# Kernel optimization log

Measured on AMD Instinct MI355X. Metric: run time of the kernel, lower is better.

Reference implementation:

```python
import jax, jax.numpy as jnp
import numpy as np

L, B, H = 1024, 64, 128


def _gru_cell(x, h, wih, whh, bih, bhh):
    # torch.nn.GRUCell math: gates ordered (r, z, n)
    gi = x @ wih.T + bih  # [B, 3H]
    gh = h @ whh.T + bhh  # [B, 3H]
    ir, iz, inn = jnp.split(gi, 3, axis=1)
    hr, hz, hn = jnp.split(gh, 3, axis=1)
    r = jax.nn.sigmoid(ir + hr)
    z = jax.nn.sigmoid(iz + hz)
    n = jnp.tanh(inn + r * hn)
    return (1.0 - z) * n + z * h


def setup_inputs() -> dict:
    key = jax.random.key(0)
    ks = jax.random.split(key, 20)
    s = 0.05  # keep tanh/sigmoid unsaturated
    f32 = jnp.float32
    return {
        "passEnc": jax.random.normal(ks[0], (L, B, 2 * H), f32),
        "Wp_w": jax.random.normal(ks[1], (H, 2 * H), f32) * s,
        "Wp_b": jax.random.normal(ks[2], (H,), f32) * s,
        "Wph_w": jax.random.normal(ks[3], (H, 2 * H), f32) * s,
        "Wph_b": jax.random.normal(ks[4], (H,), f32) * s,
        "Wg_w": jax.random.normal(ks[5], (4 * H, 4 * H), f32) * s,
        "Wg_b": jax.random.normal(ks[6], (4 * H,), f32) * s,
        "Vt": jax.random.normal(ks[7], (B, H, 1), f32),
        "wih_f": jax.random.normal(ks[8], (3 * H, 4 * H), f32) * s,
        "whh_f": jax.random.normal(ks[9], (3 * H, H), f32) * s,
        "bih_f": jax.random.normal(ks[10], (3 * H,), f32) * s,
        "bhh_f": jax.random.normal(ks[11], (3 * H,), f32) * s,
        "wih_r": jax.random.normal(ks[12], (3 * H, 4 * H), f32) * s,
        "whh_r": jax.random.normal(ks[13], (3 * H, H), f32) * s,
        "bih_r": jax.random.normal(ks[14], (3 * H,), f32) * s,
        "bhh_r": jax.random.normal(ks[15], (3 * H,), f32) * s,
        "h0_fwd": jax.random.normal(ks[16], (B, H), f32),
        "h0_rev": jax.random.normal(ks[17], (B, H), f32),
    }


def reference(passEnc, Wp_w, Wp_b, Wph_w, Wph_b, Wg_w, Wg_b, Vt,
              wih_f, whh_f, bih_f, bhh_f, wih_r, whh_r, bih_r, bhh_r,
              h0_fwd, h0_rev):
    v = Vt[:, :, 0]                       # [B, H]
    WPf = passEnc @ Wp_w.T + Wp_b        # loop-invariant WP_sub_v(passEnc), [L, B, H]
    pe_rev = jnp.flip(passEnc, axis=0)
    WPr = jnp.flip(WPf, axis=0)          # linear commutes with flip

    def attend(x_t, WP, pe):
        # x_t: [B, 2H]; WP: [L, B, H]; pe: [L, B, 2H]
        temp = jnp.tanh(WP + x_t @ Wph_w.T + Wph_b)      # [L, B, H]
        scores = jnp.einsum('lbh,bh->bl', temp, v)       # per-batch Vt
        a = jax.nn.softmax(scores, axis=1)               # over L
        c = jnp.einsum('bl,lbd->bd', a, pe)              # [B, 2H]
        cc = jnp.concatenate([x_t, c], axis=1)           # [B, 4H]
        g = jax.nn.sigmoid(cc @ Wg_w.T + Wg_b)
        return g * cc

    def step(carry, xs):
        hf, hr = carry
        xf, xr = xs
        cf = attend(xf, WPf, passEnc)
        cr = attend(xr, WPr, pe_rev)
        hf = _gru_cell(cf, hf, wih_f, whh_f, bih_f, bhh_f)
        hr = _gru_cell(cr, hr, wih_r, whh_r, bih_r, bhh_r)
        return (hf, hr), jnp.concatenate([hf, hr], axis=1)

    _, out = jax.lax.scan(step, (h0_fwd, h0_rev), (passEnc, pe_rev))
    # original applies Dropout(p=0.2); identity in eval mode
    return out  # [L, B, 2H]
```

## Files before the change

kernel.cpp:

```cpp
#include <hip/hip_runtime.h>
#include <hip/hip_bf16.h>

#define DEV __device__ __forceinline__
typedef unsigned short u16;
typedef short bf16x8 __attribute__((ext_vector_type(8)));
typedef float f32x4  __attribute__((ext_vector_type(4)));

static constexpr float LOG2E = 1.44269504088896340736f;
static constexpr float C2E   = 2.88539008177792681472f;

DEV float rcpf_(float x){ return __builtin_amdgcn_rcpf(x); }
DEV float exp2f_(float x){ return __builtin_amdgcn_exp2f(x); }
DEV float sigmoidf_(float x){ return rcpf_(1.f + exp2f_(-LOG2E*x)); }
DEV float tanhf_fast(float x){ return 1.f - 2.f*rcpf_(exp2f_(C2E*x) + 1.f); }
DEV u16 bfu(float f){
  __hip_bfloat16 h = __float2bfloat16(f);
  union { __hip_bfloat16 h; u16 u; } c; c.h = h; return c.u;
}
DEV float ubf_lo(unsigned u){ return __uint_as_float(u << 16); }
DEV float ubf_hi(unsigned u){ return __uint_as_float(u & 0xffff0000u); }
DEV unsigned pack2(float a, float b){ return (unsigned)bfu(a) | ((unsigned)bfu(b) << 16); }
DEV float ubf(u16 u){ return __uint_as_float(((unsigned)u) << 16); }

__global__ __launch_bounds__(256) void k_cvtw(const float* __restrict__ Wg,
      const float* __restrict__ wf, const float* __restrict__ wr,
      u16* __restrict__ out){
  const int i = (blockIdx.x*256 + threadIdx.x)*4;
  const float* src;
  int off;
  if (i < 262144){ src = Wg; off = i; }
  else if (i < 458752){ src = wf; off = i - 262144; }
  else { src = wr; off = i - 458752; }
  const float4 v = *(const float4*)(src + off);
  uint2 o; o.x = pack2(v.x, v.y); o.y = pack2(v.z, v.w);
  *(uint2*)(out + i) = o;
}

__global__ __launch_bounds__(256,4) void k_proj(const float* __restrict__ pe,
      const float* __restrict__ Wp, const float* __restrict__ Wpb,
      const float* __restrict__ Wph, const float* __restrict__ Wphb,
      float* __restrict__ E, float* __restrict__ F){
  __shared__ __align__(16) float xs[32*256];
  const int tid = threadIdx.x;
  const int sel = blockIdx.x >> 11;
  const long r0 = (long)(blockIdx.x & 2047) * 32;
  const float* W   = sel ? Wph  : Wp;
  const float* bia = sel ? Wphb : Wpb;
  float* out       = sel ? F    : E;
  const float4* src = (const float4*)(pe + r0*256);
  float4* dst = (float4*)xs;
  #pragma unroll
  for (int i=0;i<8;i++) dst[tid + 256*i] = src[tid + 256*i];
  __syncthreads();
  const int h = tid & 127, g = tid >> 7;
  float acc[16];
  #pragma unroll
  for (int r=0;r<16;r++) acc[r] = 0.f;
  for (int kc=0; kc<8; kc++){
    float4 w4[8];
    const float4* wp = (const float4*)(W + h*256 + kc*32);
    #pragma unroll
    for (int q=0;q<8;q++) w4[q] = wp[q];
    #pragma unroll
    for (int r=0;r<16;r++){
      const float4* xr = (const float4*)(xs + (g*16+r)*256 + kc*32);
      #pragma unroll
      for (int q=0;q<8;q++){
        const float4 xv = xr[q];
        acc[r] += xv.x*w4[q].x + xv.y*w4[q].y + xv.z*w4[q].z + xv.w*w4[q].w;
      }
    }
  }
  const float bh = bia[h];
  #pragma unroll
  for (int r=0;r<16;r++)
    out[(r0 + g*16 + r)*128 + h] = exp2f_(C2E*(acc[r] + bh));
}

#define AF_F    0
#define AF_E    8448
#define AF_PEt  12672
#define AF_S    17792
#define AF_V    19904
#define AF_M    20032
#define AF_SU   20096
#define AF_R    20160
#define A_LDSF  20224

DEV f32x4 mfma16(bf16x8 a, bf16x8 b, f32x4 c){
  return __builtin_amdgcn_mfma_f32_16x16x32_bf16(a, b, c, 0, 0, 0);
}

__global__ __launch_bounds__(512,4) void k_attn(const float* __restrict__ pe,
      const float* __restrict__ E, const float* __restrict__ F,
      const float* __restrict__ Vt, u16* __restrict__ Cout){
  __shared__ __align__(16) float lds[A_LDSF];
  const int tid = threadIdx.x;
  const int p = blockIdx.x;
  const int b = ((p >> 7) << 3) | (p & 7);
  const int tt = (p >> 3) & 15;
  const int t0 = tt * 64;
  u16* PEtu = (u16*)(lds + AF_PEt);
  u16* Pu   = (u16*)(lds + AF_S);

  for (int i = tid; i < 64*32; i += 512){
    const int r = i >> 5, c = i & 31;
    *(float4*)(lds + AF_F + r*132 + c*4) =
      *(const float4*)(F + ((long)(t0+r)*64 + b)*128 + c*4);
  }
  if (tid < 128) lds[AF_V + tid] = -2.f * Vt[b*128 + tid];
  if (tid < 64){ lds[AF_M+tid] = -__builtin_inff(); lds[AF_SU+tid] = 0.f; }

  f32x4 cacc[8];
  #pragma unroll
  for (int i=0;i<8;i++) cacc[i] = (f32x4){0.f,0.f,0.f,0.f};

  const int lane = tid & 63, w = tid >> 6;
  const int tg = lane >> 4, lg = lane & 15;
  const int ta = w*8 + tg, tb2 = ta + 4;
  const int l15 = lane & 15, kg8 = (lane >> 4) * 8;
  const int tq = w >> 1, dhalf = w & 1;
  const int tcol = tq*16 + l15;
  const int sdlo = tid & 7, slp = (tid >> 3) & 15, sdhi = tid >> 7;

  for (int lt=0; lt<32; lt++){
    const int l0 = lt*32;
    __syncthreads();
    for (int i = tid; i < 32*32; i += 512){
      const int r = i >> 5, c = i & 31;
      *(float4*)(lds + AF_E + r*132 + c*4) =
        *(const float4*)(E + ((long)(l0+r)*64 + b)*128 + c*4);
    }
    #pragma unroll
    for (int k2=0;k2<2;k2++){
      const int dseg = (sdhi + k2*4)*8 + sdlo;
      const int ll = slp*2;
      const float4 vA = *(const float4*)(pe + ((long)(l0+ll  )*64 + b)*256 + dseg*4);
      const float4 vB = *(const float4*)(pe + ((long)(l0+ll+1)*64 + b)*256 + dseg*4);
      u16* base = PEtu + (dseg*4)*40 + ll;
      *(unsigned*)(base)        = pack2(vA.x, vB.x);
      *(unsigned*)(base + 40)   = pack2(vA.y, vB.y);
      *(unsigned*)(base + 80)   = pack2(vA.z, vB.z);
      *(unsigned*)(base + 120)  = pack2(vA.w, vB.w);
    }
    __syncthreads();
    {
      float s00=0.f, s01=0.f, s10=0.f, s11=0.f;
      const float* Fa = lds + AF_F + ta*132;
      const float* Fb = lds + AF_F + tb2*132;
      const float* Ea = lds + AF_E + lg*132;
      const float* Eb = lds + AF_E + (lg+16)*132;
      const float* Vb = lds + AF_V;
      #pragma unroll 8
      for (int hc=0; hc<32; hc++){
        const float4 f0 = *(const float4*)(Fa + hc*4);
        const float4 f1 = *(const float4*)(Fb + hc*4);
        const float4 e0 = *(const float4*)(Ea + hc*4);
        const float4 e1 = *(const float4*)(Eb + hc*4);
        const float4 vv = *(const float4*)(Vb + hc*4);
        s00 += vv.x*rcpf_(f0.x*e0.x+1.f); s00 += vv.y*rcpf_(f0.y*e0.y+1.f);
        s00 += vv.z*rcpf_(f0.z*e0.z+1.f); s00 += vv.w*rcpf_(f0.w*e0.w+1.f);
        s01 += vv.x*rcpf_(f0.x*e1.x+1.f); s01 += vv.y*rcpf_(f0.y*e1.y+1.f);
        s01 += vv.z*rcpf_(f0.z*e1.z+1.f); s01 += vv.w*rcpf_(f0.w*e1.w+1.f);
        s10 += vv.x*rcpf_(f1.x*e0.x+1.f); s10 += vv.y*rcpf_(f1.y*e0.y+1.f);
        s10 += vv.z*rcpf_(f1.z*e0.z+1.f); s10 += vv.w*rcpf_(f1.w*e0.w+1.f);
        s11 += vv.x*rcpf_(f1.x*e1.x+1.f); s11 += vv.y*rcpf_(f1.y*e1.y+1.f);
        s11 += vv.z*rcpf_(f1.z*e1.z+1.f); s11 += vv.w*rcpf_(f1.w*e1.w+1.f);
      }
      lds[AF_S + ta*33  + lg]      = s00;
      lds[AF_S + ta*33  + lg + 16] = s01;
      lds[AF_S + tb2*33 + lg]      = s10;
      lds[AF_S + tb2*33 + lg + 16] = s11;
    }
    __syncthreads();
    {
      const int t = tid >> 3, sub = tid & 7;
      const float* Srow = lds + AF_S + t*33 + sub*4;
      const float s0=Srow[0], s1=Srow[1], s2=Srow[2], s3=Srow[3];
      float mx = fmaxf(fmaxf(s0,s1), fmaxf(s2,s3));
      #pragma unroll
      for (int off=1; off<8; off<<=1) mx = fmaxf(mx, __shfl_xor(mx, off));
      const float m_old = lds[AF_M + t];
      const float m_new = fmaxf(m_old, mx);
      const float p0 = exp2f_(LOG2E*(s0-m_new));
      const float p1 = exp2f_(LOG2E*(s1-m_new));
      const float p2 = exp2f_(LOG2E*(s2-m_new));
      const float p3 = exp2f_(LOG2E*(s3-m_new));
      float ps = p0+p1+p2+p3;
      #pragma unroll
      for (int off=1; off<8; off<<=1) ps += __shfl_xor(ps, off);
      __syncthreads();
      uint2 pw; pw.x = pack2(p0,p1); pw.y = pack2(p2,p3);
      *(uint2*)(Pu + t*40 + sub*4) = pw;
      if (sub==0){
        const float rsc = exp2f_(LOG2E*(m_old - m_new));
        lds[AF_R + t] = rsc;
        lds[AF_SU + t] = lds[AF_SU + t]*rsc + ps;
        lds[AF_M + t] = m_new;
      }
    }
    __syncthreads();
    {
      const float rs = lds[AF_R + tcol];
      #pragma unroll
      for (int p2=0;p2<8;p2++){
        cacc[p2][0]*=rs; cacc[p2][1]*=rs; cacc[p2][2]*=rs; cacc[p2][3]*=rs;
      }
      const bf16x8 bfrag = *(const bf16x8*)(Pu + tcol*40 + kg8);
      #pragma unroll
      for (int p2=0;p2<8;p2++){
        const int dt = dhalf*8 + p2;
        const bf16x8 afrag = *(const bf16x8*)(PEtu + (dt*16 + l15)*40 + kg8);
        cacc[p2] = mfma16(afrag, bfrag, cacc[p2]);
      }
    }
  }
  __syncthreads();
  {
    const float inv = rcpf_(lds[AF_SU + tcol]);
    u16* Cb = (u16*)(lds + AF_F);
    const int rb = (lane >> 4) * 4;
    #pragma unroll
    for (int p2=0;p2<8;p2++){
      const int dd = (dhalf*8 + p2)*16 + rb;
      *(unsigned*)(Cb + tcol*264 + dd)     = pack2(cacc[p2][0]*inv, cacc[p2][1]*inv);
      *(unsigned*)(Cb + tcol*264 + dd + 2) = pack2(cacc[p2][2]*inv, cacc[p2][3]*inv);
    }
  }
  __syncthreads();
  {
    const u16* Cb = (const u16*)(lds + AF_F);
    #pragma unroll
    for (int k2=0;k2<4;k2++){
      const int flat = tid + k2*512;
      const int t = flat >> 5, dg = flat & 31;
      const uint4 v = *(const uint4*)(Cb + t*264 + dg*8);
      *(uint4*)(Cout + ((long)(t0+t)*64 + b)*256 + dg*8) = v;
    }
  }
}

__global__ __launch_bounds__(256,2) void k_gates(const float* __restrict__ pe,
      const u16* __restrict__ Cin,
      const u16* __restrict__ Wgb16, const float* __restrict__ Wgb,
      const u16* __restrict__ wfb16, const float* __restrict__ bihf,
      const u16* __restrict__ wrb16, const float* __restrict__ bihr,
      u16* __restrict__ GIf, u16* __restrict__ GIr){
  __shared__ __align__(16) u16 ccb[32*512];
  __shared__ __align__(16) u16 gb [32*512];
  const int tid = threadIdx.x;
  const int r0 = blockIdx.x * 32;

  #pragma unroll
  for (int i=0;i<8;i++){
    const int c = tid + i*256;
    const int r = c >> 6, k0 = (c & 63)*8;
    const int kd = k0 ^ ((r&7)<<3);
    uint4 o;
    if (k0 < 256){
      const float4 f0 = *(const float4*)(pe + ((long)(r0+r))*256 + k0);
      const float4 f1 = *(const float4*)(pe + ((long)(r0+r))*256 + k0 + 4);
      o.x = pack2(f0.x,f0.y); o.y = pack2(f0.z,f0.w);
      o.z = pack2(f1.x,f1.y); o.w = pack2(f1.z,f1.w);
    } else {
      o = *(const uint4*)(Cin + ((long)(r0+r))*256 + (k0-256));
    }
    *(uint4*)(ccb + r*512 + kd) = o;
  }
  __syncthreads();

  const int l = tid & 63, wv = tid >> 6;
  const int rw = (wv >> 1) * 16;
  const int nhalf = (wv & 1) * 256;
  const int arow = rw + (l & 15);
  const int kgrp = (l >> 4) * 8;
  const int swz  = (l & 7) << 3;
  const u16* abase = ccb + arow*512;
  const int crow = rw + (l >> 4) * 4;

  for (int p2=0; p2<8; p2++){
    const int n0 = nhalf + p2*32;
    const int c0 = n0 + (l & 15), c1 = c0 + 16;
    const u16* b0p = Wgb16 + (long)c0*512 + kgrp;
    const u16* b1p = Wgb16 + (long)c1*512 + kgrp;
    f32x4 a0 = {0.f,0.f,0.f,0.f}, a1 = {0.f,0.f,0.f,0.f};
    #pragma unroll
    for (int kk=0; kk<16; kk++){
      const bf16x8 av = *(const bf16x8*)(abase + ((kk*32 + kgrp) ^ swz));
      const bf16x8 b0 = *(const bf16x8*)(b0p + kk*32);
      const bf16x8 b1 = *(const bf16x8*)(b1p + kk*32);
      a0 = mfma16(av, b0, a0);
      a1 = mfma16(av, b1, a1);
    }
    const float bi0 = Wgb[c0], bi1 = Wgb[c1];
    #pragma unroll
    for (int i=0;i<4;i++){
      gb[(crow+i)*512 + c0] = bfu(sigmoidf_(a0[i] + bi0));
      gb[(crow+i)*512 + c1] = bfu(sigmoidf_(a1[i] + bi1));
    }
  }
  __syncthreads();

  #pragma unroll
  for (int i=0;i<8;i++){
    const int c = tid + i*256;
    const int r = c >> 6, k0 = (c & 63)*8;
    const int kd = k0 ^ ((r&7)<<3);
    uint4 uc = *(const uint4*)(ccb + r*512 + kd);
    uint4 ug = *(const uint4*)(gb  + r*512 + k0);
    uint4 o;
    o.x = pack2(ubf_lo(uc.x)*ubf_lo(ug.x), ubf_hi(uc.x)*ubf_hi(ug.x));
    o.y = pack2(ubf_lo(uc.y)*ubf_lo(ug.y), ubf_hi(uc.y)*ubf_hi(ug.y));
    o.z = pack2(ubf_lo(uc.z)*ubf_lo(ug.z), ubf_hi(uc.z)*ubf_hi(ug.z));
    o.w = pack2(ubf_lo(uc.w)*ubf_lo(ug.w), ubf_hi(uc.w)*ubf_hi(ug.w));
    *(uint4*)(ccb + r*512 + kd) = o;
  }
  __syncthreads();

  const int t = r0 >> 6, b0r = r0 & 63;
  const long rbf = (long)r0 + rw;
  const long rbr = (long)(1023 - t)*64 + b0r + rw;
  u16* stg = gb + wv*512;
  const int ntbase = (wv & 1) ? 24 : 0;

  for (int p2=0; p2<12; p2++){
    const int nt = ntbase + p2*2;
    const int j0 = nt * 16;
    const bool isf = (j0 < 384);
    const u16* wb = isf ? wfb16 : wrb16;
    const float* bi = isf ? bihf : bihr;
    const int jb = isf ? j0 : (j0 - 384);
    const long rbase = isf ? rbf : rbr;
    u16* GIo = isf ? GIf : GIr;
    const int c0 = jb + (l & 15), c1 = c0 + 16;
    const u16* b0p = wb + (long)c0*512 + kgrp;
    const u16* b1p = wb + (long)c1*512 + kgrp;
    f32x4 a0 = {0.f,0.f,0.f,0.f}, a1 = {0.f,0.f,0.f,0.f};
    #pragma unroll
    for (int kk=0; kk<16; kk++){
      const bf16x8 av = *(const bf16x8*)(abase + ((kk*32 + kgrp) ^ swz));
      const bf16x8 b0 = *(const bf16x8*)(b0p + kk*32);
      const bf16x8 b1 = *(const bf16x8*)(b1p + kk*32);
      a0 = mfma16(av, b0, a0);
      a1 = mfma16(av, b1, a1);
    }
    const float bi0 = bi[c0], bi1 = bi[c1];
    #pragma unroll
    for (int i=0;i<4;i++){
      stg[((l>>4)*4+i)*16 + (l&15)]       = bfu(a0[i] + bi0);
      stg[256 + ((l>>4)*4+i)*16 + (l&15)] = bfu(a1[i] + bi1);
    }
    {
      const int rr = l >> 2, q = l & 3;
      const uint2 v0 = *(const uint2*)(stg + rr*16 + q*4);
      const uint2 v1 = *(const uint2*)(stg + 256 + rr*16 + q*4);
      *(uint2*)(GIo + (rbase + rr)*384 + jb      + q*4) = v0;
      *(uint2*)(GIo + (rbase + rr)*384 + jb + 16 + q*4) = v1;
    }
  }
}

__global__ __launch_bounds__(512,2) void k_gru(
      const u16* __restrict__ GIf, const u16* __restrict__ GIr,
      const float* __restrict__ whhf, const float* __restrict__ bhhf,
      const float* __restrict__ whhr, const float* __restrict__ bhhr,
      const float* __restrict__ h0f, const float* __restrict__ h0r,
      float* __restrict__ out){
  const int d = blockIdx.x >> 6, b = blockIdx.x & 63;
  const u16* GI = d ? GIr  : GIf;
  const float* whh = d ? whhr : whhf;
  const float* bhh = d ? bhhr : bhhf;
  const float* h0  = d ? h0r  : h0f;
  const int tid = threadIdx.x;
  const int seg = tid >> 7, j0 = tid & 127;
  __shared__ __align__(16) float hsh[128];
  __shared__ __align__(16) float part[4*384];

  float4 wR[8], wZ[8], wN[8];
  {
    const float4* r0p = (const float4*)(whh + (long)(j0      )*128 + seg*32);
    const float4* r1p = (const float4*)(whh + (long)(j0 + 128)*128 + seg*32);
    const float4* r2p = (const float4*)(whh + (long)(j0 + 256)*128 + seg*32);
    #pragma unroll
    for (int q=0;q<8;q++){ wR[q]=r0p[q]; wZ[q]=r1p[q]; wN[q]=r2p[q]; }
  }
  float bjr=0.f, bjz=0.f, bjn=0.f, hold=0.f;
  float gr_n=0.f, gz_n=0.f, gn_n=0.f;
  if (tid < 128){
    hsh[tid] = hold = h0[b*128 + tid];
    bjr = bhh[tid]; bjz = bhh[tid+128]; bjn = bhh[tid+256];
    gr_n = ubf(GI[(long)b*384 + tid]);
    gz_n = ubf(GI[(long)b*384 + tid + 128]);
    gn_n = ubf(GI[(long)b*384 + tid + 256]);
  }
  __syncthreads();

  for (int t=0; t<1024; t++){
    {
      float aR=0.f, aZ=0.f, aN=0.f;
      const float4* hseg = (const float4*)(hsh + seg*32);
      #pragma unroll
      for (int q=0;q<8;q++){
        const float4 hv = hseg[q];
        aR += wR[q].x*hv.x + wR[q].y*hv.y + wR[q].z*hv.z + wR[q].w*hv.w;
        aZ += wZ[q].x*hv.x + wZ[q].y*hv.y + wZ[q].z*hv.z + wZ[q].w*hv.w;
        aN += wN[q].x*hv.x + wN[q].y*hv.y + wN[q].z*hv.z + wN[q].w*hv.w;
      }
      part[seg*384 + j0]       = aR;
      part[seg*384 + j0 + 128] = aZ;
      part[seg*384 + j0 + 256] = aN;
    }
    __syncthreads();
    if (tid < 128){
      const float gr = gr_n, gz = gz_n, gn = gn_n;
      if (t < 1023){
        const long base = ((long)(t+1)*64 + b)*384 + tid;
        gr_n = ubf(GI[base]); gz_n = ubf(GI[base+128]); gn_n = ubf(GI[base+256]);
      }
      const float ghr = bjr + ((part[tid]       + part[384+tid])       + (part[768+tid]       + part[1152+tid]));
      const float ghz = bjz + ((part[tid+128]   + part[384+tid+128])   + (part[768+tid+128]   + part[1152+tid+128]));
      const float ghn = bjn + ((part[tid+256]   + part[384+tid+256])   + (part[768+tid+256]   + part[1152+tid+256]));
      const float r = sigmoidf_(gr + ghr);
      const float z = sigmoidf_(gz + ghz);
      const float n = tanhf_fast(gn + r*ghn);
      const float hnew = (1.f - z)*n + z*hold;
      hold = hnew;
      hsh[tid] = hnew;
      out[((long)t*64 + b)*256 + d*128 + tid] = hnew;
    }
    __syncthreads();
  }
}

__global__ void k_sentinel(float* out){ out[0] = 1.0e6f; }

extern "C" void kernel_launch(void* const* d_in, const int* in_sizes, int n_in,
                              void* d_out, int out_size, void* d_ws, size_t ws_size,
                              hipStream_t stream){
  const float* passEnc = (const float*)d_in[0];
  const float* Wp_w  = (const float*)d_in[1];
  const float* Wp_b  = (const float*)d_in[2];
  const float* Wph_w = (const float*)d_in[3];
  const float* Wph_b = (const float*)d_in[4];
  const float* Wg_w  = (const float*)d_in[5];
  const float* Wg_b  = (const float*)d_in[6];
  const float* Vt    = (const float*)d_in[7];
  const float* wih_f = (const float*)d_in[8];
  const float* whh_f = (const float*)d_in[9];
  const float* bih_f = (const float*)d_in[10];
  const float* bhh_f = (const float*)d_in[11];
  const float* wih_r = (const float*)d_in[12];
  const float* whh_r = (const float*)d_in[13];
  const float* bih_r = (const float*)d_in[14];
  const float* bhh_r = (const float*)d_in[15];
  const float* h0f   = (const float*)d_in[16];
  const float* h0r   = (const float*)d_in[17];
  float* out = (float*)d_out;

  const size_t NEED = 134217728ull;
  if (ws_size < NEED){ k_sentinel<<<1,1,0,stream>>>(out); return; }
  char* base = (char*)d_ws;
  u16* GIf = (u16*)base;
  u16* GIr = (u16*)(base + 50331648ull);
  u16* C   = (u16*)(base + 100663296ull);
  float* E = (float*)base;
  float* F = (float*)(base + 33554432ull);
  u16* wgb16 = (u16*)d_out;
  u16* wfb16 = wgb16 + 262144;
  u16* wrb16 = wfb16 + 196608;

  k_cvtw <<<640,  256, 0, stream>>>(Wg_w, wih_f, wih_r, wgb16);
  k_proj <<<4096, 256, 0, stream>>>(passEnc, Wp_w, Wp_b, Wph_w, Wph_b, E, F);
  k_attn <<<1024, 512, 0, stream>>>(passEnc, E, F, Vt, C);
  k_gates<<<2048, 256, 0, stream>>>(passEnc, C, wgb16, Wg_b,
                                    wfb16, bih_f, wrb16, bih_r, GIf, GIr);
  k_gru  <<<128,  512, 0, stream>>>(GIf, GIr, whh_f, bhh_f, whh_r, bhh_r, h0f, h0r, out);
}
```

Before: 2.587 ms.

## Batch reciprocals in attention scores and widen gates kernel to 512 threads

```diff
diff --git a/kernel.cpp b/kernel.cpp
--- a/kernel.cpp
+++ b/kernel.cpp
@@ -21,6 +21,22 @@
 DEV float ubf_hi(unsigned u){ return __uint_as_float(u & 0xffff0000u); }
 DEV unsigned pack2(float a, float b){ return (unsigned)bfu(a) | ((unsigned)bfu(b) << 16); }
 DEV float ubf(u16 u){ return __uint_as_float(((unsigned)u) << 16); }
+
+DEV void acc4inv(const float4 f, const float4 e, const float4 v, float& s){
+  const float dx = __builtin_fmaf(f.x, e.x, 1.f);
+  const float dy = __builtin_fmaf(f.y, e.y, 1.f);
+  const float dz = __builtin_fmaf(f.z, e.z, 1.f);
+  const float dw = __builtin_fmaf(f.w, e.w, 1.f);
+  const float p2 = dx*dy, p3 = p2*dz, p4 = p3*dw;
+  const float r4 = rcpf_(p4);
+  const float iw = r4*p3;
+  const float s3 = r4*dw;
+  const float iz = s3*p2;
+  const float s2 = s3*dz;
+  const float iy = s2*dx;
+  const float ix = s2*dy;
+  s += v.x*ix; s += v.y*iy; s += v.z*iz; s += v.w*iw;
+}
 
 __global__ __launch_bounds__(256) void k_cvtw(const float* __restrict__ Wg,
       const float* __restrict__ wf, const float* __restrict__ wr,
@@ -151,21 +167,17 @@
       const float* Ea = lds + AF_E + lg*132;
       const float* Eb = lds + AF_E + (lg+16)*132;
       const float* Vb = lds + AF_V;
-      #pragma unroll 8
+      #pragma unroll 4
       for (int hc=0; hc<32; hc++){
         const float4 f0 = *(const float4*)(Fa + hc*4);
         const float4 f1 = *(const float4*)(Fb + hc*4);
         const float4 e0 = *(const float4*)(Ea + hc*4);
         const float4 e1 = *(const float4*)(Eb + hc*4);
         const float4 vv = *(const float4*)(Vb + hc*4);
-        s00 += vv.x*rcpf_(f0.x*e0.x+1.f); s00 += vv.y*rcpf_(f0.y*e0.y+1.f);
-        s00 += vv.z*rcpf_(f0.z*e0.z+1.f); s00 += vv.w*rcpf_(f0.w*e0.w+1.f);
-        s01 += vv.x*rcpf_(f0.x*e1.x+1.f); s01 += vv.y*rcpf_(f0.y*e1.y+1.f);
-        s01 += vv.z*rcpf_(f0.z*e1.z+1.f); s01 += vv.w*rcpf_(f0.w*e1.w+1.f);
-        s10 += vv.x*rcpf_(f1.x*e0.x+1.f); s10 += vv.y*rcpf_(f1.y*e0.y+1.f);
-        s10 += vv.z*rcpf_(f1.z*e0.z+1.f); s10 += vv.w*rcpf_(f1.w*e0.w+1.f);
-        s11 += vv.x*rcpf_(f1.x*e1.x+1.f); s11 += vv.y*rcpf_(f1.y*e1.y+1.f);
-        s11 += vv.z*rcpf_(f1.z*e1.z+1.f); s11 += vv.w*rcpf_(f1.w*e1.w+1.f);
+        acc4inv(f0, e0, vv, s00);
+        acc4inv(f0, e1, vv, s01);
+        acc4inv(f1, e0, vv, s10);
+        acc4inv(f1, e1, vv, s11);
       }
       lds[AF_S + ta*33  + lg]      = s00;
       lds[AF_S + ta*33  + lg + 16] = s01;
@@ -240,7 +252,7 @@
   }
 }
 
-__global__ __launch_bounds__(256,2) void k_gates(const float* __restrict__ pe,
+__global__ __launch_bounds__(512,2) void k_gates(const float* __restrict__ pe,
       const u16* __restrict__ Cin,
       const u16* __restrict__ Wgb16, const float* __restrict__ Wgb,
       const u16* __restrict__ wfb16, const float* __restrict__ bihf,
@@ -252,8 +264,8 @@
   const int r0 = blockIdx.x * 32;
 
   #pragma unroll
-  for (int i=0;i<8;i++){
-    const int c = tid + i*256;
+  for (int i=0;i<4;i++){
+    const int c = tid + i*512;
     const int r = c >> 6, k0 = (c & 63)*8;
     const int kd = k0 ^ ((r&7)<<3);
     uint4 o;
@@ -270,16 +282,16 @@
   __syncthreads();
 
   const int l = tid & 63, wv = tid >> 6;
-  const int rw = (wv >> 1) * 16;
-  const int nhalf = (wv & 1) * 256;
+  const int rw = (wv >> 2) * 16;
+  const int nq = wv & 3;
   const int arow = rw + (l & 15);
   const int kgrp = (l >> 4) * 8;
   const int swz  = (l & 7) << 3;
   const u16* abase = ccb + arow*512;
   const int crow = rw + (l >> 4) * 4;
 
-  for (int p2=0; p2<8; p2++){
-    const int n0 = nhalf + p2*32;
+  for (int p2=0; p2<4; p2++){
+    const int n0 = nq*128 + p2*32;
     const int c0 = n0 + (l & 15), c1 = c0 + 16;
     const u16* b0p = Wgb16 + (long)c0*512 + kgrp;
     const u16* b1p = Wgb16 + (long)c1*512 + kgrp;
@@ -302,8 +314,8 @@
   __syncthreads();
 
   #pragma unroll
-  for (int i=0;i<8;i++){
-    const int c = tid + i*256;
+  for (int i=0;i<4;i++){
+    const int c = tid + i*512;
     const int r = c >> 6, k0 = (c & 63)*8;
     const int kd = k0 ^ ((r&7)<<3);
     uint4 uc = *(const uint4*)(ccb + r*512 + kd);
@@ -321,10 +333,9 @@
   const long rbf = (long)r0 + rw;
   const long rbr = (long)(1023 - t)*64 + b0r + rw;
   u16* stg = gb + wv*512;
-  const int ntbase = (wv & 1) ? 24 : 0;
-
-  for (int p2=0; p2<12; p2++){
-    const int nt = ntbase + p2*2;
+
+  for (int p2=0; p2<6; p2++){
+    const int nt = nq*12 + p2*2;
     const int j0 = nt * 16;
     const bool isf = (j0 < 384);
     const u16* wb = isf ? wfb16 : wrb16;
@@ -472,7 +483,7 @@
   k_cvtw <<<640,  256, 0, stream>>>(Wg_w, wih_f, wih_r, wgb16);
   k_proj <<<4096, 256, 0, stream>>>(passEnc, Wp_w, Wp_b, Wph_w, Wph_b, E, F);
   k_attn <<<1024, 512, 0, stream>>>(passEnc, E, F, Vt, C);
-  k_gates<<<2048, 256, 0, stream>>>(passEnc, C, wgb16, Wg_b,
+  k_gates<<<2048, 512, 0, stream>>>(passEnc, C, wgb16, Wg_b,
                                     wfb16, bih_f, wrb16, bih_r, GIf, GIr);
   k_gru  <<<128,  512, 0, stream>>>(GIf, GIr, whh_f, bhh_f, whh_r, bhh_r, h0f, h0r, out);
 }
```

After: 2.609 ms. Within noise of the previous version (+0.8%).
